# Optimization experiments

Hardware: AMD Instinct MI355X
Metric: run time of the kernel (lower is better)

Reference implementation:

```python
import jax, jax.numpy as jnp
import numpy as np

NUM_EXPERTS = 8
TOP_K = 2
HIDDEN = 2048
INTER = 1408
TOKENS = 4096


def setup_inputs() -> dict:
    key = jax.random.key(0)
    ks = jax.random.split(key, 5)
    scale_h = 1.0 / np.sqrt(HIDDEN)
    scale_i = 1.0 / np.sqrt(INTER)
    return {
        "x": jax.random.normal(ks[0], (TOKENS, HIDDEN), dtype=jnp.float32),
        "router_w": jax.random.normal(ks[1], (NUM_EXPERTS, HIDDEN), dtype=jnp.float32) * scale_h,
        "w_gate": jax.random.normal(ks[2], (NUM_EXPERTS, HIDDEN, INTER), dtype=jnp.float32) * scale_h,
        "w_up": jax.random.normal(ks[3], (NUM_EXPERTS, HIDDEN, INTER), dtype=jnp.float32) * scale_h,
        "w_down": jax.random.normal(ks[4], (NUM_EXPERTS, INTER, HIDDEN), dtype=jnp.float32) * scale_i,
    }


def reference(x, router_w, w_gate, w_up, w_down):
    # Router: softmax over experts, top-k, renormalize top-k probs
    logits = x @ router_w.T                       # [T, E]
    probs = jax.nn.softmax(logits, axis=-1)
    top_vals, top_idx = jax.lax.top_k(probs, TOP_K)  # [T, K]
    top_vals = top_vals / jnp.sum(top_vals, axis=-1, keepdims=True)
    # Combine weights: [T, E], zero for unselected experts
    t_ar = jnp.arange(x.shape[0])[:, None]
    combine = jnp.zeros((x.shape[0], NUM_EXPERTS), dtype=x.dtype).at[t_ar, top_idx].add(top_vals)
    # Expert SwiGLU FFN: down( silu(x@gate) * (x@up) ), weighted combine.
    # Loop over the small fixed expert set (8); each iteration is a dense GEMM chain.
    out = jnp.zeros_like(x)
    for e in range(NUM_EXPERTS):
        h = jax.nn.silu(x @ w_gate[e]) * (x @ w_up[e])  # [T, INTER]
        out = out + combine[:, e:e + 1] * (h @ w_down[e])
    return out
```

## Files before the change

kernel.cpp:

```cpp
#include <hip/hip_runtime.h>
#include <hip/hip_bf16.h>
#include <cstdint>
#include <cstddef>

#define TOKENS 4096
#define HIDDEN 2048
#define INTER  1408
#define NE     8
#define NGU    2816
#define CAP_ROWS 9216

typedef __bf16 bf16;
typedef __bf16 bf16x8 __attribute__((ext_vector_type(8)));
typedef __bf16 bf16x4 __attribute__((ext_vector_type(4)));
typedef float  f32x4  __attribute__((ext_vector_type(4)));

__device__ __forceinline__ void async16(const void* g, void* l) {
  __builtin_amdgcn_global_load_lds((const __attribute__((address_space(1))) void*)g,
                                   (__attribute__((address_space(3))) void*)l,
                                   16, 0, 0);
}

__global__ void router_kernel(const float* __restrict__ x, const float* __restrict__ rw,
                              bf16* __restrict__ xb, int* __restrict__ cnt,
                              int* __restrict__ tok, float* __restrict__ wts,
                              int* __restrict__ inv) {
  const int w = threadIdx.x >> 6, l = threadIdx.x & 63;
  const int t = blockIdx.x * 4 + w;
  const float4* x4 = (const float4*)(x + (size_t)t * HIDDEN);
  const float4* r4 = (const float4*)rw;
  float acc[NE];
#pragma unroll
  for (int e = 0; e < NE; ++e) acc[e] = 0.f;
#pragma unroll
  for (int c = 0; c < 8; ++c) {
    const int idx = c * 64 + l;
    const float4 v = x4[idx];
    bf16* dst = xb + (size_t)t * HIDDEN + idx * 4;
    dst[0] = (bf16)v.x; dst[1] = (bf16)v.y; dst[2] = (bf16)v.z; dst[3] = (bf16)v.w;
#pragma unroll
    for (int e = 0; e < NE; ++e) {
      const float4 u = r4[e * 512 + idx];
      acc[e] += v.x * u.x + v.y * u.y + v.z * u.z + v.w * u.w;
    }
  }
#pragma unroll
  for (int e = 0; e < NE; ++e)
#pragma unroll
    for (int s = 32; s > 0; s >>= 1) acc[e] += __shfl_xor(acc[e], s, 64);
  if (l == 0) {
    int i0 = 0; float l0 = acc[0];
#pragma unroll
    for (int e = 1; e < NE; ++e) if (acc[e] > l0) { l0 = acc[e]; i0 = e; }
    int i1 = -1; float l1 = -3.4e38f;
#pragma unroll
    for (int e = 0; e < NE; ++e) if (e != i0 && acc[e] > l1) { l1 = acc[e]; i1 = e; }
    const float w0 = 1.f / (1.f + __expf(l1 - l0));
    const float w1 = 1.f - w0;
    int p = atomicAdd(&cnt[i0], 1);
    tok[i0 * 4096 + p] = t; wts[i0 * 4096 + p] = w0; inv[t * 2]     = (i0 << 12) | p;
    p = atomicAdd(&cnt[i1], 1);
    tok[i1 * 4096 + p] = t; wts[i1 * 4096 + p] = w1; inv[t * 2 + 1] = (i1 << 12) | p;
  }
}

__global__ void scan_kernel(const int* __restrict__ cnt, int* __restrict__ offs) {
  if (threadIdx.x == 0 && blockIdx.x == 0) {
    int o = 0;
    for (int e = 0; e < NE; ++e) { offs[e] = o; o += ((cnt[e] + 127) >> 7) << 7; }
    offs[NE] = o;
  }
}

__global__ __launch_bounds__(256) void prep_weights(
    const float* __restrict__ wg, const float* __restrict__ wu, const float* __restrict__ wd,
    bf16* __restrict__ wgu, bf16* __restrict__ wdt) {
  __shared__ float tile[64][65];
  const int bid = blockIdx.x;
  const int which = bid / 5632;
  const int rem = bid - which * 5632;
  const int e = rem & 7;
  const int tid2 = rem >> 3;
  const float* in; bf16* out; int R, C, c0, r0, mode;
  if (which == 2) {
    in = wd + (size_t)e * INTER * HIDDEN; out = wdt + (size_t)e * HIDDEN * INTER;
    R = INTER; C = HIDDEN; c0 = (tid2 & 31) * 64; r0 = (tid2 >> 5) * 64; mode = 0;
  } else {
    in = (which ? wu : wg) + (size_t)e * HIDDEN * INTER; out = wgu + (size_t)e * NGU * HIDDEN;
    R = HIDDEN; C = INTER; c0 = (tid2 % 22) * 64; r0 = (tid2 / 22) * 64; mode = which + 1;
  }
  const int t = threadIdx.x;
  const int row = t >> 4, cq = t & 15;
  const float* src = in + (size_t)(r0 + row) * C + c0 + cq * 4;
#pragma unroll
  for (int p = 0; p < 4; ++p) {
    const float4 v = *(const float4*)(src + (size_t)(p * 16) * C);
    *(float4*)&tile[p * 16 + row][cq * 4] = v;
  }
  __syncthreads();
  const int oc = t >> 2, rq = t & 3;
  float vals[16];
#pragma unroll
  for (int i = 0; i < 16; ++i) vals[i] = tile[rq * 16 + i][oc];
  const int c = c0 + oc;
  int p;
  if (mode == 0) p = c;
  else p = ((c >> 4) << 5) + (c & 15) + (mode == 2 ? 16 : 0);
  bf16x8 o0, o1;
#pragma unroll
  for (int i = 0; i < 8; ++i) { o0[i] = (bf16)vals[i]; o1[i] = (bf16)vals[8 + i]; }
  bf16* dst = out + (size_t)p * R + r0 + rq * 16;
  *(bf16x8*)dst = o0;
  *(bf16x8*)(dst + 8) = o1;
}

__global__ __launch_bounds__(256, 4) void gemm_gateup(
    const bf16* __restrict__ X, const bf16* __restrict__ W, bf16* __restrict__ H,
    const int* __restrict__ cnt, const int* __restrict__ offs,
    const int* __restrict__ tok, const float* __restrict__ wts) {
  const int e = blockIdx.x & 7;
  const int slot = blockIdx.x >> 3;
  const int c = cnt[e];
  if (c == 0) return;
  const int mtiles = (c + 127) >> 7;
  const int total = mtiles * (NGU / 128);

  __shared__ bf16 sA[2 * 128 * 32];
  __shared__ bf16 sB[2 * 128 * 32];

  const int t = threadIdx.x, l = t & 63, w = t >> 6;
  const int iA0 = t, iA1 = t + 256;
  const int rA0 = iA0 >> 2, g0 = iA0 & 3;
  const int rA1 = iA1 >> 2, g1 = iA1 & 3;
  bf16* la0 = sA + iA0 * 8; bf16* la1 = sA + iA1 * 8;
  bf16* lb0 = sB + iA0 * 8; bf16* lb1 = sB + iA1 * 8;

  const int wm = (w >> 1) * 64, wn = (w & 1) * 64;
  const int r16 = l & 15, quad = l >> 4;
  const bf16* fA = sA + (wm + r16) * 32 + quad * 8;
  const bf16* fB = sB + (wn + r16) * 32 + quad * 8;

  for (int it = slot; it < total; it += 256) {
    const int mt = it % mtiles;
    const int nt = it / mtiles;

    const int gr0 = tok[e * 4096 + (mt * 128 + rA0 < c ? mt * 128 + rA0 : c - 1)];
    const int gr1 = tok[e * 4096 + (mt * 128 + rA1 < c ? mt * 128 + rA1 : c - 1)];
    const bf16* pa0 = X + (size_t)gr0 * HIDDEN + g0 * 8;
    const bf16* pa1 = X + (size_t)gr1 * HIDDEN + g1 * 8;
    const bf16* pb0 = W + ((size_t)e * NGU + nt * 128 + rA0) * HIDDEN + g0 * 8;
    const bf16* pb1 = W + ((size_t)e * NGU + nt * 128 + rA1) * HIDDEN + g1 * 8;

    f32x4 acc[4][4];
#pragma unroll
    for (int i = 0; i < 4; ++i)
#pragma unroll
      for (int j = 0; j < 4; ++j) acc[i][j] = (f32x4){0.f, 0.f, 0.f, 0.f};

    for (int kk = 0; kk < HIDDEN; kk += 64) {
      async16(pa0 + kk, la0);       async16(pa1 + kk, la1);
      async16(pb0 + kk, lb0);       async16(pb1 + kk, lb1);
      async16(pa0 + kk + 32, la0 + 4096); async16(pa1 + kk + 32, la1 + 4096);
      async16(pb0 + kk + 32, lb0 + 4096); async16(pb1 + kk + 32, lb1 + 4096);
      __syncthreads();
#pragma unroll
      for (int sf = 0; sf < 2; ++sf) {
        bf16x8 a[4], b[4];
#pragma unroll
        for (int i = 0; i < 4; ++i) a[i] = *(const bf16x8*)(fA + sf * 4096 + i * 16 * 32);
#pragma unroll
        for (int j = 0; j < 4; ++j) b[j] = *(const bf16x8*)(fB + sf * 4096 + j * 16 * 32);
#pragma unroll
        for (int i = 0; i < 4; ++i)
#pragma unroll
          for (int j = 0; j < 4; ++j)
            acc[i][j] = __builtin_amdgcn_mfma_f32_16x16x32_bf16(b[j], a[i], acc[i][j], 0, 0, 0);
      }
      __syncthreads();
    }

    const int mRowBase = mt * 128 + wm + r16;
    const int hcolBase = nt * 64 + (wn >> 1) + quad * 4;
#pragma unroll
    for (int i = 0; i < 4; ++i) {
      const int m = mRowBase + i * 16;
      const int mc = m < c ? m : c - 1;
      const float ws = wts[e * 4096 + mc];
      bf16* rowp = H + (size_t)(offs[e] + m) * INTER;
#pragma unroll
      for (int jp = 0; jp < 2; ++jp) {
        bf16x4 hv;
#pragma unroll
        for (int r = 0; r < 4; ++r) {
          const float g = acc[i][2 * jp][r];
          const float u = acc[i][2 * jp + 1][r];
          hv[r] = (bf16)((g / (1.f + __expf(-g))) * u * ws);
        }
        *(bf16x4*)(rowp + hcolBase + jp * 16) = hv;
      }
    }
  }
}

__global__ __launch_bounds__(256, 4) void gemm_down(
    const bf16* __restrict__ Hin, const bf16* __restrict__ W, float* __restrict__ ybuf,
    const int* __restrict__ cnt, const int* __restrict__ offs) {
  const int e = blockIdx.x & 7;
  const int slot = blockIdx.x >> 3;
  const int c = cnt[e];
  if (c == 0) return;
  const int mtiles = (c + 127) >> 7;
  const int total = mtiles * (HIDDEN / 128);

  __shared__ bf16 sA[2 * 128 * 32];
  __shared__ bf16 sB[2 * 128 * 32];

  const int t = threadIdx.x, l = t & 63, w = t >> 6;
  const int iA0 = t, iA1 = t + 256;
  const int rA0 = iA0 >> 2, g0 = iA0 & 3;
  const int rA1 = iA1 >> 2, g1 = iA1 & 3;
  bf16* la0 = sA + iA0 * 8; bf16* la1 = sA + iA1 * 8;
  bf16* lb0 = sB + iA0 * 8; bf16* lb1 = sB + iA1 * 8;

  const int wm = (w >> 1) * 64, wn = (w & 1) * 64;
  const int r16 = l & 15, quad = l >> 4;
  const bf16* fA = sA + (wm + r16) * 32 + quad * 8;
  const bf16* fB = sB + (wn + r16) * 32 + quad * 8;

  for (int it = slot; it < total; it += 256) {
    const int mt = it % mtiles;
    const int nt = it / mtiles;

    const int base = offs[e] + mt * 128;
    const bf16* pa0 = Hin + (size_t)(base + rA0) * INTER + g0 * 8;
    const bf16* pa1 = Hin + (size_t)(base + rA1) * INTER + g1 * 8;
    const bf16* pb0 = W + ((size_t)e * HIDDEN + nt * 128 + rA0) * INTER + g0 * 8;
    const bf16* pb1 = W + ((size_t)e * HIDDEN + nt * 128 + rA1) * INTER + g1 * 8;

    f32x4 acc[4][4];
#pragma unroll
    for (int i = 0; i < 4; ++i)
#pragma unroll
      for (int j = 0; j < 4; ++j) acc[i][j] = (f32x4){0.f, 0.f, 0.f, 0.f};

    for (int kk = 0; kk < INTER; kk += 64) {
      async16(pa0 + kk, la0);       async16(pa1 + kk, la1);
      async16(pb0 + kk, lb0);       async16(pb1 + kk, lb1);
      async16(pa0 + kk + 32, la0 + 4096); async16(pa1 + kk + 32, la1 + 4096);
      async16(pb0 + kk + 32, lb0 + 4096); async16(pb1 + kk + 32, lb1 + 4096);
      __syncthreads();
#pragma unroll
      for (int sf = 0; sf < 2; ++sf) {
        bf16x8 a[4], b[4];
#pragma unroll
        for (int i = 0; i < 4; ++i) a[i] = *(const bf16x8*)(fA + sf * 4096 + i * 16 * 32);
#pragma unroll
        for (int j = 0; j < 4; ++j) b[j] = *(const bf16x8*)(fB + sf * 4096 + j * 16 * 32);
#pragma unroll
        for (int i = 0; i < 4; ++i)
#pragma unroll
          for (int j = 0; j < 4; ++j)
            acc[i][j] = __builtin_amdgcn_mfma_f32_16x16x32_bf16(b[j], a[i], acc[i][j], 0, 0, 0);
      }
      __syncthreads();
    }

    const int mRowBase = mt * 128 + wm + r16;
    const int colBase = nt * 128 + wn + quad * 4;
#pragma unroll
    for (int i = 0; i < 4; ++i) {
      const int m = mRowBase + i * 16;
      if (m < c) {
        float* rowp = ybuf + (size_t)(offs[e] + m) * HIDDEN + colBase;
#pragma unroll
        for (int j = 0; j < 4; ++j)
          *(f32x4*)(rowp + j * 16) = acc[i][j];
      }
    }
  }
}

__global__ __launch_bounds__(256) void combine_kernel(
    const float* __restrict__ y, const int* __restrict__ inv,
    const int* __restrict__ offs, float* __restrict__ out) {
  const int idx = blockIdx.x * 256 + threadIdx.x;
  const int tkn = idx >> 9, q = idx & 511;
  const int v0 = inv[tkn * 2], v1 = inv[tkn * 2 + 1];
  const size_t r0 = (size_t)(offs[v0 >> 12] + (v0 & 4095));
  const size_t r1 = (size_t)(offs[v1 >> 12] + (v1 & 4095));
  const float4 a = ((const float4*)y)[r0 * 512 + q];
  const float4 b = ((const float4*)y)[r1 * 512 + q];
  float4 o; o.x = a.x + b.x; o.y = a.y + b.y; o.z = a.z + b.z; o.w = a.w + b.w;
  ((float4*)out)[idx] = o;
}

extern "C" void kernel_launch(void* const* d_in, const int* in_sizes, int n_in,
                              void* d_out, int out_size, void* d_ws, size_t ws_size,
                              hipStream_t stream) {
  const float* x  = (const float*)d_in[0];
  const float* rw = (const float*)d_in[1];
  const float* wg = (const float*)d_in[2];
  const float* wu = (const float*)d_in[3];
  const float* wd = (const float*)d_in[4];
  float* out = (float*)d_out;

  char* ws = (char*)d_ws;
  size_t o = 0;
  auto alloc = [&](size_t b) { void* p = ws + o; o += (b + 255) & ~(size_t)255; return p; };
  int*   cnt  = (int*)alloc(NE * 4);
  int*   offs = (int*)alloc((NE + 1) * 4);
  int*   tok  = (int*)alloc((size_t)NE * 4096 * 4);
  float* wts  = (float*)alloc((size_t)NE * 4096 * 4);
  int*   inv  = (int*)alloc((size_t)TOKENS * 2 * 4);
  bf16*  xb   = (bf16*)alloc((size_t)TOKENS * HIDDEN * 2);
  bf16*  wgu  = (bf16*)alloc((size_t)NE * NGU * HIDDEN * 2);
  bf16*  wdt  = (bf16*)alloc((size_t)NE * HIDDEN * INTER * 2);
  bf16*  h    = (bf16*)alloc((size_t)CAP_ROWS * INTER * 2);
  float* ybuf = (float*)wgu;

  hipMemsetAsync(cnt, 0, NE * 4, stream);

  router_kernel<<<TOKENS / 4, 256, 0, stream>>>(x, rw, xb, cnt, tok, wts, inv);
  scan_kernel<<<1, 64, 0, stream>>>(cnt, offs);

  prep_weights<<<dim3(3 * 5632), 256, 0, stream>>>(wg, wu, wd, wgu, wdt);

  gemm_gateup<<<dim3(2048), 256, 0, stream>>>(xb, wgu, h, cnt, offs, tok, wts);
  gemm_down<<<dim3(2048), 256, 0, stream>>>(h, wdt, ybuf, cnt, offs);
  combine_kernel<<<dim3(TOKENS * (HIDDEN / 4) / 256), 256, 0, stream>>>(
      ybuf, inv, offs, out);
}
```

Measured before the change: 652.9 us.

## Double-buffer LDS k-slices with vmcnt waits to overlap loads with MFMA

Both expert GEMM kernels change their K loop from load-all-then-compute over 64-wide chunks into a two-stage pipeline over 32-wide slices. The next slice's async global-to-LDS loads are issued while the current slice is consumed, and partial s_waitcnt vmcnt(4) waits replace full syncthreads drains. The goal is to hide global memory latency behind MFMA work. In exchange it adds two barriers per 32-wide step and relies on hand-written waitcnt and sched_barrier placement being correct.

Result: no change. 654.6 us (+0.3%).

```diff
diff --git a/kernel.cpp b/kernel.cpp
--- a/kernel.cpp
+++ b/kernel.cpp
@@ -20,6 +20,9 @@
                                    (__attribute__((address_space(3))) void*)l,
                                    16, 0, 0);
 }
+
+#define WAIT_VM4() do { asm volatile("s_waitcnt vmcnt(4)" ::: "memory"); } while (0)
+#define WAIT_VM0() do { asm volatile("s_waitcnt vmcnt(0)" ::: "memory"); } while (0)
 
 __global__ void router_kernel(const float* __restrict__ x, const float* __restrict__ rw,
                               bf16* __restrict__ xb, int* __restrict__ cnt,
@@ -157,26 +160,42 @@
 #pragma unroll
       for (int j = 0; j < 4; ++j) acc[i][j] = (f32x4){0.f, 0.f, 0.f, 0.f};
 
-    for (int kk = 0; kk < HIDDEN; kk += 64) {
-      async16(pa0 + kk, la0);       async16(pa1 + kk, la1);
-      async16(pb0 + kk, lb0);       async16(pb1 + kk, lb1);
-      async16(pa0 + kk + 32, la0 + 4096); async16(pa1 + kk + 32, la1 + 4096);
-      async16(pb0 + kk + 32, lb0 + 4096); async16(pb1 + kk + 32, lb1 + 4096);
-      __syncthreads();
-#pragma unroll
-      for (int sf = 0; sf < 2; ++sf) {
-        bf16x8 a[4], b[4];
-#pragma unroll
-        for (int i = 0; i < 4; ++i) a[i] = *(const bf16x8*)(fA + sf * 4096 + i * 16 * 32);
-#pragma unroll
-        for (int j = 0; j < 4; ++j) b[j] = *(const bf16x8*)(fB + sf * 4096 + j * 16 * 32);
-#pragma unroll
-        for (int i = 0; i < 4; ++i)
-#pragma unroll
-          for (int j = 0; j < 4; ++j)
-            acc[i][j] = __builtin_amdgcn_mfma_f32_16x16x32_bf16(b[j], a[i], acc[i][j], 0, 0, 0);
+    async16(pa0, la0);           async16(pa1, la1);
+    async16(pb0, lb0);           async16(pb1, lb1);
+    async16(pa0 + 32, la0 + 4096); async16(pa1 + 32, la1 + 4096);
+    async16(pb0 + 32, lb0 + 4096); async16(pb1 + 32, lb1 + 4096);
+    WAIT_VM4();
+    __builtin_amdgcn_sched_barrier(0);
+    __builtin_amdgcn_s_barrier();
+
+    const int nk = HIDDEN / 32;
+    int cur = 0;
+    for (int tt = 0; tt < nk; ++tt) {
+      const int co = cur * 4096;
+      bf16x8 a[4], b[4];
+#pragma unroll
+      for (int i = 0; i < 4; ++i) a[i] = *(const bf16x8*)(fA + co + i * 16 * 32);
+#pragma unroll
+      for (int j = 0; j < 4; ++j) b[j] = *(const bf16x8*)(fB + co + j * 16 * 32);
+#pragma unroll
+      for (int i = 0; i < 4; ++i)
+#pragma unroll
+        for (int j = 0; j < 4; ++j)
+          acc[i][j] = __builtin_amdgcn_mfma_f32_16x16x32_bf16(b[j], a[i], acc[i][j], 0, 0, 0);
+      __builtin_amdgcn_sched_barrier(0);
+      __builtin_amdgcn_s_barrier();
+      if (tt + 2 < nk) {
+        const int kk = (tt + 2) * 32;
+        const int so = cur * 4096;
+        async16(pa0 + kk, la0 + so); async16(pa1 + kk, la1 + so);
+        async16(pb0 + kk, lb0 + so); async16(pb1 + kk, lb1 + so);
+        WAIT_VM4();
+      } else {
+        WAIT_VM0();
       }
-      __syncthreads();
+      __builtin_amdgcn_sched_barrier(0);
+      __builtin_amdgcn_s_barrier();
+      cur ^= 1;
     }
 
     const int mRowBase = mt * 128 + wm + r16;
@@ -243,26 +262,42 @@
 #pragma unroll
       for (int j = 0; j < 4; ++j) acc[i][j] = (f32x4){0.f, 0.f, 0.f, 0.f};
 
-    for (int kk = 0; kk < INTER; kk += 64) {
-      async16(pa0 + kk, la0);       async16(pa1 + kk, la1);
-      async16(pb0 + kk, lb0);       async16(pb1 + kk, lb1);
-      async16(pa0 + kk + 32, la0 + 4096); async16(pa1 + kk + 32, la1 + 4096);
-      async16(pb0 + kk + 32, lb0 + 4096); async16(pb1 + kk + 32, lb1 + 4096);
-      __syncthreads();
-#pragma unroll
-      for (int sf = 0; sf < 2; ++sf) {
-        bf16x8 a[4], b[4];
-#pragma unroll
-        for (int i = 0; i < 4; ++i) a[i] = *(const bf16x8*)(fA + sf * 4096 + i * 16 * 32);
-#pragma unroll
-        for (int j = 0; j < 4; ++j) b[j] = *(const bf16x8*)(fB + sf * 4096 + j * 16 * 32);
-#pragma unroll
-        for (int i = 0; i < 4; ++i)
-#pragma unroll
-          for (int j = 0; j < 4; ++j)
-            acc[i][j] = __builtin_amdgcn_mfma_f32_16x16x32_bf16(b[j], a[i], acc[i][j], 0, 0, 0);
+    async16(pa0, la0);           async16(pa1, la1);
+    async16(pb0, lb0);           async16(pb1, lb1);
+    async16(pa0 + 32, la0 + 4096); async16(pa1 + 32, la1 + 4096);
+    async16(pb0 + 32, lb0 + 4096); async16(pb1 + 32, lb1 + 4096);
+    WAIT_VM4();
+    __builtin_amdgcn_sched_barrier(0);
+    __builtin_amdgcn_s_barrier();
+
+    const int nk = INTER / 32;
+    int cur = 0;
+    for (int tt = 0; tt < nk; ++tt) {
+      const int co = cur * 4096;
+      bf16x8 a[4], b[4];
+#pragma unroll
+      for (int i = 0; i < 4; ++i) a[i] = *(const bf16x8*)(fA + co + i * 16 * 32);
+#pragma unroll
+      for (int j = 0; j < 4; ++j) b[j] = *(const bf16x8*)(fB + co + j * 16 * 32);
+#pragma unroll
+      for (int i = 0; i < 4; ++i)
+#pragma unroll
+        for (int j = 0; j < 4; ++j)
+          acc[i][j] = __builtin_amdgcn_mfma_f32_16x16x32_bf16(b[j], a[i], acc[i][j], 0, 0, 0);
+      __builtin_amdgcn_sched_barrier(0);
+      __builtin_amdgcn_s_barrier();
+      if (tt + 2 < nk) {
+        const int kk = (tt + 2) * 32;
+        const int so = cur * 4096;
+        async16(pa0 + kk, la0 + so); async16(pa1 + kk, la1 + so);
+        async16(pb0 + kk, lb0 + so); async16(pb1 + kk, lb1 + so);
+        WAIT_VM4();
+      } else {
+        WAIT_VM0();
       }
-      __syncthreads();
+      __builtin_amdgcn_sched_barrier(0);
+      __builtin_amdgcn_s_barrier();
+      cur ^= 1;
     }
 
     const int mRowBase = mt * 128 + wm + r16;
```
